# Kernel tuning notes

Hardware: AMD Instinct MI355X
Metric: run time of the kernel (lower is better)

Reference implementation:

```python
import jax, jax.numpy as jnp
import numpy as np

TIME_SEG_LEN = 5
PRED_STEPS = 1
B, N, D = 4, 4096, 4
F1, F2 = 32, 64  # cnn filters; F2 must equal GCSConv/Dense width 64


def _conv1d_time(x, Wc1, bc1, Wc2, bc2):
    # x: [B, N, T, D] -> per-node temporal CNN collapsing T=5 -> 1 -> [B, N, F2]
    b, n, t, d = x.shape
    xr = x.reshape(b * n, t, d)
    dn = ('NWC', 'WIO', 'NWC')
    h = jax.lax.conv_general_dilated(xr, Wc1, (1,), 'VALID', dimension_numbers=dn) + bc1
    h = jax.nn.relu(h)
    h = jax.lax.conv_general_dilated(h, Wc2, (1,), 'VALID', dimension_numbers=dn) + bc2
    return h.reshape(b, n, -1)  # [B, N, F2]


def setup_inputs() -> dict:
    key = jax.random.key(0)
    ks = jax.random.split(key, 12)
    time_segs = jax.random.normal(ks[0], (B, TIME_SEG_LEN, N, D), dtype=jnp.float32)
    edges = jax.random.randint(ks[1], (N, N), 0, 2, dtype=jnp.int32)
    s = lambda *sh: 1.0 / np.sqrt(sh[-2] if len(sh) > 1 else sh[0])
    return {
        'time_segs': time_segs,
        'edges': edges,
        'Wc1': jax.random.normal(ks[2], (3, D, F1), dtype=jnp.float32) * 0.3,
        'bc1': jnp.zeros((F1,), jnp.float32),
        'Wc2': jax.random.normal(ks[3], (3, F1, F2), dtype=jnp.float32) * 0.1,
        'bc2': jnp.zeros((F2,), jnp.float32),
        'Wg1': jax.random.normal(ks[4], (F2, 64), dtype=jnp.float32) * 0.125,
        'bg': jnp.zeros((64,), jnp.float32),
        'Wd': jax.random.normal(ks[5], (F2 + 64, 64), dtype=jnp.float32) * 0.09,
        'bd': jnp.zeros((64,), jnp.float32),
        'Wo': jax.random.normal(ks[6], (64, D), dtype=jnp.float32) * 0.125,
        'bo': jnp.zeros((D,), jnp.float32),
    }


def reference(time_segs, edges, Wc1, bc1, Wc2, bc2, Wg1, bg, Wd, bd, Wo, bo):
    A = edges.astype(jnp.float32)
    n = A.shape[0]
    deg = jnp.sum(A, axis=-1, keepdims=True)              # row degree
    A_norm = A / jnp.where(deg > 0, deg, 1.0)             # D^-1 A (symmetric=False)
    A_nd = A_norm * (1.0 - jnp.eye(n, dtype=A.dtype))     # self-edge masking of X row j == zeroing diag
    col_deg = jnp.sum(A, axis=0)                          # e = np.sum(edges, axis=0)
    alive = (col_deg != 0).astype(time_segs.dtype)[None, :, None]  # zero-degree nodes -> zeros branch

    ext = jnp.transpose(time_segs, (0, 2, 1, 3))          # [B, N, T, D]
    for i in range(PRED_STEPS):
        seg = ext[:, :, i:, :]                            # [B, N, 5, D]
        cond = _conv1d_time(seg, Wc1, bc1, Wc2, bc2)      # [B, N, F2]
        # Vectorized per-node masked GCSConv: row j of tanh(A X_j W1 + X_j W2 + b)
        # with X_j = X zeroed at node j. Skip term vanishes at row j.
        agg = jnp.einsum('jk,bkf->bjf', A_nd, cond)       # [B, N, F2]
        G = jnp.tanh(agg @ Wg1 + bg) * alive              # [B, N, 64]
        h = jax.nn.relu(jnp.concatenate([cond, G], axis=-1) @ Wd + bd)
        nxt = seg[:, :, -1, :] + jnp.tanh(h @ Wo + bo)    # residual update [B, N, D]
        ext = jnp.concatenate([ext, nxt[:, :, None, :]], axis=2)
    out = jnp.transpose(ext, (0, 2, 1, 3))                # [B, T+P, N, D]
    return out[:, TIME_SEG_LEN:, :, :]                    # [B, pred_steps, N, D]
```

## Files before the change

kernel.cpp:

```cpp
#include <hip/hip_runtime.h>
#include <math.h>

typedef unsigned short ushort_t;
typedef unsigned int uint_t;
typedef unsigned long long u64_t;
typedef __attribute__((ext_vector_type(8))) __bf16 bf16x8;
typedef __attribute__((ext_vector_type(4))) float f32x4;

#define NN 4096
#define TT 5
#define F1 32
#define F2 64

__device__ __forceinline__ ushort_t f2bf(float x) {
    union { float f; uint_t u; } v; v.f = x;
    uint_t r = (v.u + 0x7FFFu + ((v.u >> 16) & 1u)) >> 16;
    return (ushort_t)r;
}
__device__ __forceinline__ float bf16f(float x) {
    union { float f; uint_t u; } v; v.f = x;
    v.u = (v.u + 0x7FFFu + ((v.u >> 16) & 1u)) & 0xFFFF0000u;
    return v.f;
}
__device__ __forceinline__ uint_t pk2(float a, float b) {
    return (uint_t)f2bf(a) | ((uint_t)f2bf(b) << 16);
}
__device__ __forceinline__ float tanh_fast(float x) {
    const float xc = fminf(fmaxf(x, -10.f), 10.f);
    const float e = __expf(2.f * xc);
    return (e - 1.f) * __builtin_amdgcn_rcpf(e + 1.f);
}

#define H1S 104
#define CBS 80
__global__ __launch_bounds__(256) void k1_cond(
    const float* __restrict__ ts, const float* __restrict__ Wc1, const float* __restrict__ bc1,
    const float* __restrict__ Wc2, const float* __restrict__ bc2,
    float* __restrict__ condf, ushort_t* __restrict__ condT)
{
    const int b = blockIdx.y;
    const int j0 = blockIdx.x * 64;
    const int t = threadIdx.x;

    __shared__ float sWc1[384];
    __shared__ float sbc1[F1];
    __shared__ float sbc2[F2];
    __shared__ ushort_t sWc2T[64 * H1S];
    __shared__ ushort_t h1B[64 * H1S];
    __shared__ ushort_t scb[64 * CBS];

    for (int i = t; i < 384; i += 256) sWc1[i] = Wc1[i];
    if (t < F1) sbc1[t] = bc1[t];
    if (t < F2) sbc2[t] = bc2[t];
    for (int i = t; i < 96 * 64; i += 256) {
        const int e = i >> 6, f = i & 63;
        sWc2T[f * H1S + e] = f2bf(Wc2[i]);
    }
    __syncthreads();

    {
        const int n = t & 63, f10 = (t >> 6) * 8;
        const int j = j0 + n;
        float4 x[5];
        #pragma unroll
        for (int tt = 0; tt < 5; ++tt)
            x[tt] = *(const float4*)(ts + ((((size_t)b * TT + tt) << 12) + j) * 4);
        #pragma unroll
        for (int tt0 = 0; tt0 < 3; ++tt0) {
            #pragma unroll
            for (int ff = 0; ff < 8; ++ff) {
                const int f1 = f10 + ff;
                float a = sbc1[f1];
                #pragma unroll
                for (int dt = 0; dt < 3; ++dt) {
                    const float4 xx = x[tt0 + dt];
                    a += xx.x * sWc1[(dt * 4 + 0) * F1 + f1];
                    a += xx.y * sWc1[(dt * 4 + 1) * F1 + f1];
                    a += xx.z * sWc1[(dt * 4 + 2) * F1 + f1];
                    a += xx.w * sWc1[(dt * 4 + 3) * F1 + f1];
                }
                h1B[n * H1S + tt0 * 32 + f1] = f2bf(fmaxf(a, 0.f));
            }
        }
    }
    __syncthreads();

    {
        const int w = t >> 6, l = t & 63;
        const int m0 = w * 16, kseg = (l >> 4) * 8;
        f32x4 acc[4] = {};
        #pragma unroll
        for (int ks = 0; ks < 3; ++ks) {
            const bf16x8 av = *(const bf16x8*)&h1B[(m0 + (l & 15)) * H1S + ks * 32 + kseg];
            #pragma unroll
            for (int ct = 0; ct < 4; ++ct) {
                const bf16x8 bv = *(const bf16x8*)&sWc2T[(ct * 16 + (l & 15)) * H1S + ks * 32 + kseg];
                acc[ct] = __builtin_amdgcn_mfma_f32_16x16x32_bf16(av, bv, acc[ct], 0, 0, 0);
            }
        }
        #pragma unroll
        for (int ct = 0; ct < 4; ++ct)
            #pragma unroll
            for (int i = 0; i < 4; ++i) {
                const int row = m0 + (l >> 4) * 4 + i;
                const int col = ct * 16 + (l & 15);
                const float c = acc[ct][i] + sbc2[col];
                condf[((((size_t)b << 12) + j0 + row) << 6) + col] = c;
                scb[col * CBS + row] = f2bf(c);
            }
    }
    __syncthreads();
    {
        const int f2 = t >> 2, seg = t & 3;
        ushort_t* dst = condT + (((size_t)b * 64 + f2) << 12) + j0 + seg * 16;
        *(uint4*)dst = *(const uint4*)&scb[f2 * CBS + seg * 16];
        *(uint4*)(dst + 8) = *(const uint4*)&scb[f2 * CBS + seg * 16 + 8];
    }
}

__device__ __forceinline__ void stage_chunk(
    const int4 pa, int it, int kq, ushort_t* dstbuf, int soff, uint_t& regm, int& cnt)
{
    const u64_t b0 = __ballot(pa.x != 0);
    const u64_t b1 = __ballot(pa.y != 0);
    const u64_t b2 = __ballot(pa.z != 0);
    const u64_t b3 = __ballot(pa.w != 0);
    const uint_t m0 = (uint_t)(b0 | (b0 >> 32)), m1 = (uint_t)(b1 | (b1 >> 32));
    const uint_t m2 = (uint_t)(b2 | (b2 >> 32)), m3 = (uint_t)(b3 | (b3 >> 32));
    const uint_t nib = ((m0 >> kq) & 1u) | (((m1 >> kq) & 1u) << 1) |
                       (((m2 >> kq) & 1u) << 2) | (((m3 >> kq) & 1u) << 3);
    regm |= nib << (it * 4);
    cnt += (pa.x != 0) + (pa.y != 0) + (pa.z != 0) + (pa.w != 0);
    const uint_t h01 = (pa.x ? 0x3F80u : 0u) | (pa.y ? 0x3F800000u : 0u);
    const uint_t h23 = (pa.z ? 0x3F80u : 0u) | (pa.w ? 0x3F800000u : 0u);
    *(uint2*)(dstbuf + soff) = make_uint2(h01, h23);
}

__global__ __launch_bounds__(1024, 8) void k3_gemm(
    const int* __restrict__ edges, const ushort_t* __restrict__ condT,
    float* __restrict__ agg0, float* __restrict__ agg1,
    float* __restrict__ agg2, float* __restrict__ agg3,
    int* __restrict__ degI, uint_t* __restrict__ colbits)
{
    const int t = threadIdx.x;
    const int stripe = blockIdx.x >> 2, ks4 = blockIdx.x & 3;
    const int j0 = stripe * 32, kb = ks4 * 1024;

    __shared__ __align__(16) ushort_t abuf[8][4096];

    const int w = t >> 6, l = t & 63;
    const int r = t >> 5, kq = t & 31;
    const int rl = r & 15, rh = r >> 4;
    const int ks_s = kq >> 3, q_s = (kq >> 1) & 3;
    const int soff = (rh * 2048 + ks_s * 512 + (q_s * 16 + rl) * 8 + (kq & 1) * 4) ^ (q_s << 4);
    const int aoff = (l * 8) ^ ((l >> 4) << 4);

    const int* ep = edges + (size_t)(j0 + r) * NN + kb + kq * 4;
    const ushort_t* bp = condT + (size_t)(w * 16 + (l & 15)) * NN + kb + (l >> 4) * 8;

    uint_t regm = 0; int cnt = 0;
    int4 pa[4];

    #pragma unroll
    for (int c = 0; c < 4; ++c) pa[c] = *(const int4*)(ep + c * 128);
    #pragma unroll
    for (int c = 0; c < 4; ++c) stage_chunk(pa[c], c, kq, &abuf[c][0], soff, regm, cnt);
    __syncthreads();

    #pragma unroll
    for (int c = 0; c < 4; ++c) pa[c] = *(const int4*)(ep + (c + 4) * 128);

    f32x4 acc0 = {0.f, 0.f, 0.f, 0.f};
    f32x4 acc1 = {0.f, 0.f, 0.f, 0.f};

    #pragma unroll
    for (int ch = 0; ch < 4; ++ch) {
        const ushort_t* ab = &abuf[ch][0];
        const ushort_t* bpi = bp + ch * 128;
        #pragma unroll
        for (int ks = 0; ks < 4; ++ks) {
            const bf16x8 bfv = *(const bf16x8*)(bpi + ks * 32);
            const bf16x8 a0 = *(const bf16x8*)(ab + ks * 512 + aoff);
            const bf16x8 a1 = *(const bf16x8*)(ab + 2048 + ks * 512 + aoff);
            acc0 = __builtin_amdgcn_mfma_f32_16x16x32_bf16(a0, bfv, acc0, 0, 0, 0);
            acc1 = __builtin_amdgcn_mfma_f32_16x16x32_bf16(a1, bfv, acc1, 0, 0, 0);
        }
    }
    #pragma unroll
    for (int c = 0; c < 4; ++c) stage_chunk(pa[c], c + 4, kq, &abuf[c + 4][0], soff, regm, cnt);
    __syncthreads();

    #pragma unroll
    for (int ch = 4; ch < 8; ++ch) {
        const ushort_t* ab = &abuf[ch][0];
        const ushort_t* bpi = bp + ch * 128;
        #pragma unroll
        for (int ks = 0; ks < 4; ++ks) {
            const bf16x8 bfv = *(const bf16x8*)(bpi + ks * 32);
            const bf16x8 a0 = *(const bf16x8*)(ab + ks * 512 + aoff);
            const bf16x8 a1 = *(const bf16x8*)(ab + 2048 + ks * 512 + aoff);
            acc0 = __builtin_amdgcn_mfma_f32_16x16x32_bf16(a0, bfv, acc0, 0, 0, 0);
            acc1 = __builtin_amdgcn_mfma_f32_16x16x32_bf16(a1, bfv, acc1, 0, 0, 0);
        }
    }

    {
        float* aggS = (ks4 == 0) ? agg0 : (ks4 == 1) ? agg1 : (ks4 == 2) ? agg2 : agg3;
        const int col = w * 16 + (l & 15);
        float* dst = aggS + ((size_t)(col >> 6) * NN << 6) + (col & 63);
        #pragma unroll
        for (int i = 0; i < 4; ++i) {
            const int ja = j0 + (l >> 4) * 4 + i;
            dst[(size_t)ja << 6] = acc0[i];
            dst[(size_t)(ja + 16) << 6] = acc1[i];
        }
    }
    {
        int s = cnt;
        #pragma unroll
        for (int off = 16; off >= 1; off >>= 1) s += __shfl_down(s, off, 32);
        if (kq == 0) atomicAdd(&degI[j0 + r], s);
    }
    __syncthreads();
    uint_t* colsh = (uint_t*)&abuf[0][0];
    if (l < 32) colsh[w * 32 + kq] = regm;
    __syncthreads();
    if (t < 32) {
        uint_t v = 0;
        #pragma unroll
        for (int w2 = 0; w2 < 16; ++w2) v |= colsh[w2 * 32 + t];
        colsh[512 + t] = v;
    }
    __syncthreads();
    if (t < 32) {
        const int it = t >> 2, koct = t & 3;
        uint_t word = 0;
        #pragma unroll
        for (int s2 = 0; s2 < 8; ++s2)
            word |= ((colsh[512 + koct * 8 + s2] >> (it * 4)) & 15u) << (s2 * 4);
        atomicOr(&colbits[(kb >> 5) + t], word);
    }
}

#define WGS 88
#define WDS 136
#define HS  69
__global__ __launch_bounds__(256) void k4_mlp(
    const float* __restrict__ ts, const int* __restrict__ edges,
    const float* __restrict__ condf,
    const float* __restrict__ agg0, const float* __restrict__ agg1,
    const float* __restrict__ agg2, const float* __restrict__ agg3,
    const int* __restrict__ degI, const uint_t* __restrict__ colbits,
    const float* __restrict__ Wg1, const float* __restrict__ bg,
    const float* __restrict__ Wd, const float* __restrict__ bd,
    const float* __restrict__ Wo, const float* __restrict__ bo,
    float* __restrict__ out)
{
    const int b = blockIdx.y;
    const int j0 = blockIdx.x * 64;
    const int t = threadIdx.x;

    __shared__ ushort_t sWg1T[64 * WGS];
    __shared__ ushort_t sWdT[64 * WDS];
    __shared__ ushort_t aggB[64 * WGS];
    __shared__ ushort_t catB[64 * WDS];
    __shared__ float sH[64 * HS];
    __shared__ float sWo[256];
    __shared__ float sbg[64], sbd[64], sbo[4], sAlive[64];

    for (int i = t; i < 4096; i += 256) {
        const int in = i >> 6, o = i & 63;
        sWg1T[o * WGS + in] = f2bf(Wg1[i]);
    }
    for (int i = t; i < 8192; i += 256) {
        const int in = i >> 6, o = i & 63;
        sWdT[o * WDS + in] = f2bf(Wd[i]);
    }
    if (t < 256) sWo[t] = Wo[t];
    if (t < 64) { sbg[t] = bg[t]; sbd[t] = bd[t]; }
    if (t < 4) sbo[t] = bo[t];
    if (t < 64) {
        const int j = j0 + t;
        sAlive[t] = (float)((colbits[j >> 5] >> (j & 31)) & 1u);
    }
    {
        const int r = t >> 2, fs = t & 3;
        const int j = j0 + r;
        const float dv = (float)degI[j];
        const float inv = 1.f / (dv > 0.f ? dv : 1.f);
        const float dgf = edges[(size_t)j * NN + j] ? 1.f : 0.f;
        const size_t base = (((size_t)b << 12) + j) << 6;
        #pragma unroll
        for (int q = 0; q < 4; ++q) {
            const int f = fs * 16 + q * 4;
            const float4 a0 = *(const float4*)(agg0 + base + f);
            const float4 a1 = *(const float4*)(agg1 + base + f);
            const float4 a2 = *(const float4*)(agg2 + base + f);
            const float4 a3 = *(const float4*)(agg3 + base + f);
            const float4 c4 = *(const float4*)(condf + base + f);
            const float n0 = (a0.x + a1.x + a2.x + a3.x - dgf * bf16f(c4.x)) * inv;
            const float n1 = (a0.y + a1.y + a2.y + a3.y - dgf * bf16f(c4.y)) * inv;
            const float n2 = (a0.z + a1.z + a2.z + a3.z - dgf * bf16f(c4.z)) * inv;
            const float n3 = (a0.w + a1.w + a2.w + a3.w - dgf * bf16f(c4.w)) * inv;
            *(uint2*)&aggB[r * WGS + f] = make_uint2(pk2(n0, n1), pk2(n2, n3));
            *(uint2*)&catB[r * WDS + f] = make_uint2(pk2(c4.x, c4.y), pk2(c4.z, c4.w));
        }
    }
    __syncthreads();

    const int w = t >> 6, l = t & 63;
    const int m0 = w * 16, kseg = (l >> 4) * 8;

    {
        f32x4 acc[4] = {};
        #pragma unroll
        for (int ks = 0; ks < 2; ++ks) {
            const bf16x8 av = *(const bf16x8*)&aggB[(m0 + (l & 15)) * WGS + ks * 32 + kseg];
            #pragma unroll
            for (int ct = 0; ct < 4; ++ct) {
                const bf16x8 bv = *(const bf16x8*)&sWg1T[(ct * 16 + (l & 15)) * WGS + ks * 32 + kseg];
                acc[ct] = __builtin_amdgcn_mfma_f32_16x16x32_bf16(av, bv, acc[ct], 0, 0, 0);
            }
        }
        #pragma unroll
        for (int ct = 0; ct < 4; ++ct)
            #pragma unroll
            for (int i = 0; i < 4; ++i) {
                const int row = m0 + (l >> 4) * 4 + i;
                const int col = ct * 16 + (l & 15);
                const float g = tanh_fast(acc[ct][i] + sbg[col]) * sAlive[row];
                catB[row * WDS + 64 + col] = f2bf(g);
            }
    }
    __syncthreads();
    {
        f32x4 acc[4] = {};
        #pragma unroll
        for (int ks = 0; ks < 4; ++ks) {
            const bf16x8 av = *(const bf16x8*)&catB[(m0 + (l & 15)) * WDS + ks * 32 + kseg];
            #pragma unroll
            for (int ct = 0; ct < 4; ++ct) {
                const bf16x8 bv = *(const bf16x8*)&sWdT[(ct * 16 + (l & 15)) * WDS + ks * 32 + kseg];
                acc[ct] = __builtin_amdgcn_mfma_f32_16x16x32_bf16(av, bv, acc[ct], 0, 0, 0);
            }
        }
        #pragma unroll
        for (int ct = 0; ct < 4; ++ct)
            #pragma unroll
            for (int i = 0; i < 4; ++i) {
                const int row = m0 + (l >> 4) * 4 + i;
                const int col = ct * 16 + (l & 15);
                sH[row * HS + col] = fmaxf(acc[ct][i] + sbd[col], 0.f);
            }
    }
    __syncthreads();
    {
        const int r = t >> 2, d = t & 3;
        const int j = j0 + r;
        float s = sbo[d];
        #pragma unroll 8
        for (int f = 0; f < 64; ++f) s += sH[r * HS + f] * sWo[f * 4 + d];
        const float segl = ts[((((size_t)b * TT + 4) << 12) + j) * 4 + d];
        out[((((size_t)b << 12) + j) << 2) + d] = segl + tanh_fast(s);
    }
}

extern "C" void kernel_launch(void* const* d_in, const int* in_sizes, int n_in,
                              void* d_out, int out_size, void* d_ws, size_t ws_size,
                              hipStream_t stream)
{
    (void)in_sizes; (void)n_in; (void)out_size; (void)ws_size;
    const float* ts    = (const float*)d_in[0];
    const int*   edges = (const int*)d_in[1];
    const float* Wc1   = (const float*)d_in[2];
    const float* bc1   = (const float*)d_in[3];
    const float* Wc2   = (const float*)d_in[4];
    const float* bc2   = (const float*)d_in[5];
    const float* Wg1   = (const float*)d_in[6];
    const float* bg    = (const float*)d_in[7];
    const float* Wd    = (const float*)d_in[8];
    const float* bd    = (const float*)d_in[9];
    const float* Wo    = (const float*)d_in[10];
    const float* bo    = (const float*)d_in[11];
    float* out = (float*)d_out;

    char* ws = (char*)d_ws;
    ushort_t* condT   = (ushort_t*)(ws);
    float*    condf   = (float*)(ws + (size_t)(2 << 20));
    float*    agg0    = (float*)(ws + (size_t)(6 << 20));
    float*    agg1    = (float*)(ws + (size_t)(10 << 20));
    float*    agg2    = (float*)(ws + (size_t)(14 << 20));
    float*    agg3    = (float*)(ws + (size_t)(18 << 20));
    int*      degI    = (int*)(ws + (size_t)(22 << 20));
    uint_t*   colbits = (uint_t*)(ws + (size_t)(22 << 20) + 16384);

    hipMemsetAsync(degI, 0, 16384 + 512, stream);

    k1_cond<<<dim3(64, 4), 256, 0, stream>>>(ts, Wc1, bc1, Wc2, bc2, condf, condT);
    k3_gemm<<<512, 1024, 0, stream>>>(edges, condT, agg0, agg1, agg2, agg3, degI, colbits);
    k4_mlp<<<dim3(64, 4), 256, 0, stream>>>(ts, edges, condf, agg0, agg1, agg2, agg3,
                                            degI, colbits, Wg1, bg, Wd, bd, Wo, bo, out);
}
```

Baseline: 164.7 us.

## Fold memset into k1, double the block sizes, and prefetch B operands in the GEMM

```diff
diff --git a/kernel.cpp b/kernel.cpp
--- a/kernel.cpp
+++ b/kernel.cpp
@@ -30,13 +30,17 @@
     const float e = __expf(2.f * xc);
     return (e - 1.f) * __builtin_amdgcn_rcpf(e + 1.f);
 }
+__device__ __forceinline__ void lds_barrier() {
+    asm volatile("s_waitcnt lgkmcnt(0)\n\ts_barrier" ::: "memory");
+}
 
 #define H1S 104
 #define CBS 80
-__global__ __launch_bounds__(256) void k1_cond(
+__global__ __launch_bounds__(512) void k1_cond(
     const float* __restrict__ ts, const float* __restrict__ Wc1, const float* __restrict__ bc1,
     const float* __restrict__ Wc2, const float* __restrict__ bc2,
-    float* __restrict__ condf, ushort_t* __restrict__ condT)
+    float* __restrict__ condf, ushort_t* __restrict__ condT,
+    int* __restrict__ degI, uint_t* __restrict__ colbits)
 {
     const int b = blockIdx.y;
     const int j0 = blockIdx.x * 64;
@@ -49,61 +53,65 @@
     __shared__ ushort_t h1B[64 * H1S];
     __shared__ ushort_t scb[64 * CBS];
 
-    for (int i = t; i < 384; i += 256) sWc1[i] = Wc1[i];
+    if (blockIdx.x == 0 && b == 0) {
+        for (int i = t; i < 4096; i += 512) degI[i] = 0;
+        if (t < 128) colbits[t] = 0u;
+    }
+
+    for (int i = t; i < 384; i += 512) sWc1[i] = Wc1[i];
     if (t < F1) sbc1[t] = bc1[t];
     if (t < F2) sbc2[t] = bc2[t];
-    for (int i = t; i < 96 * 64; i += 256) {
+    for (int i = t; i < 96 * 64; i += 512) {
         const int e = i >> 6, f = i & 63;
         sWc2T[f * H1S + e] = f2bf(Wc2[i]);
     }
     __syncthreads();
 
     {
-        const int n = t & 63, f10 = (t >> 6) * 8;
+        const int n = t & 63, g = t >> 6;
         const int j = j0 + n;
         float4 x[5];
         #pragma unroll
         for (int tt = 0; tt < 5; ++tt)
             x[tt] = *(const float4*)(ts + ((((size_t)b * TT + tt) << 12) + j) * 4);
         #pragma unroll
-        for (int tt0 = 0; tt0 < 3; ++tt0) {
-            #pragma unroll
-            for (int ff = 0; ff < 8; ++ff) {
-                const int f1 = f10 + ff;
-                float a = sbc1[f1];
-                #pragma unroll
-                for (int dt = 0; dt < 3; ++dt) {
-                    const float4 xx = x[tt0 + dt];
-                    a += xx.x * sWc1[(dt * 4 + 0) * F1 + f1];
-                    a += xx.y * sWc1[(dt * 4 + 1) * F1 + f1];
-                    a += xx.z * sWc1[(dt * 4 + 2) * F1 + f1];
-                    a += xx.w * sWc1[(dt * 4 + 3) * F1 + f1];
-                }
-                h1B[n * H1S + tt0 * 32 + f1] = f2bf(fmaxf(a, 0.f));
-            }
+        for (int q = 0; q < 12; ++q) {
+            const int e = g * 12 + q;
+            const int tt0 = e >> 5, f1 = e & 31;
+            float a = sbc1[f1];
+            #pragma unroll
+            for (int dt = 0; dt < 3; ++dt) {
+                const float4 xx = x[tt0 + dt];
+                a += xx.x * sWc1[(dt * 4 + 0) * F1 + f1];
+                a += xx.y * sWc1[(dt * 4 + 1) * F1 + f1];
+                a += xx.z * sWc1[(dt * 4 + 2) * F1 + f1];
+                a += xx.w * sWc1[(dt * 4 + 3) * F1 + f1];
+            }
+            h1B[n * H1S + e] = f2bf(fmaxf(a, 0.f));
         }
     }
     __syncthreads();
 
     {
         const int w = t >> 6, l = t & 63;
-        const int m0 = w * 16, kseg = (l >> 4) * 8;
-        f32x4 acc[4] = {};
+        const int m0 = (w & 3) * 16, cH = (w >> 2) * 32;
+        const int kseg = (l >> 4) * 8;
+        f32x4 acc[2] = {};
         #pragma unroll
         for (int ks = 0; ks < 3; ++ks) {
             const bf16x8 av = *(const bf16x8*)&h1B[(m0 + (l & 15)) * H1S + ks * 32 + kseg];
             #pragma unroll
-            for (int ct = 0; ct < 4; ++ct) {
-                const bf16x8 bv = *(const bf16x8*)&sWc2T[(ct * 16 + (l & 15)) * H1S + ks * 32 + kseg];
+            for (int ct = 0; ct < 2; ++ct) {
+                const bf16x8 bv = *(const bf16x8*)&sWc2T[(cH + ct * 16 + (l & 15)) * H1S + ks * 32 + kseg];
                 acc[ct] = __builtin_amdgcn_mfma_f32_16x16x32_bf16(av, bv, acc[ct], 0, 0, 0);
             }
         }
         #pragma unroll
-        for (int ct = 0; ct < 4; ++ct)
+        for (int ct = 0; ct < 2; ++ct)
             #pragma unroll
             for (int i = 0; i < 4; ++i) {
                 const int row = m0 + (l >> 4) * 4 + i;
-                const int col = ct * 16 + (l & 15);
+                const int col = cH + ct * 16 + (l & 15);
                 const float c = acc[ct][i] + sbc2[col];
                 condf[((((size_t)b << 12) + j0 + row) << 6) + col] = c;
                 scb[col * CBS + row] = f2bf(c);
@@ -111,10 +119,9 @@
     }
     __syncthreads();
     {
-        const int f2 = t >> 2, seg = t & 3;
-        ushort_t* dst = condT + (((size_t)b * 64 + f2) << 12) + j0 + seg * 16;
-        *(uint4*)dst = *(const uint4*)&scb[f2 * CBS + seg * 16];
-        *(uint4*)(dst + 8) = *(const uint4*)&scb[f2 * CBS + seg * 16 + 8];
+        const int f2 = t >> 3, seg = t & 7;
+        ushort_t* dst = condT + (((size_t)b * 64 + f2) << 12) + j0 + seg * 8;
+        *(uint4*)dst = *(const uint4*)&scb[f2 * CBS + seg * 8];
     }
 }
 
@@ -160,12 +167,15 @@
 
     uint_t regm = 0; int cnt = 0;
     int4 pa[4];
+    bf16x8 bcur[4], bnxt[4];
 
     #pragma unroll
     for (int c = 0; c < 4; ++c) pa[c] = *(const int4*)(ep + c * 128);
     #pragma unroll
+    for (int ks = 0; ks < 4; ++ks) bcur[ks] = *(const bf16x8*)(bp + ks * 32);
+    #pragma unroll
     for (int c = 0; c < 4; ++c) stage_chunk(pa[c], c, kq, &abuf[c][0], soff, regm, cnt);
-    __syncthreads();
+    lds_barrier();
 
     #pragma unroll
     for (int c = 0; c < 4; ++c) pa[c] = *(const int4*)(ep + (c + 4) * 128);
@@ -175,32 +185,42 @@
 
     #pragma unroll
     for (int ch = 0; ch < 4; ++ch) {
+        const ushort_t* bpn = bp + (ch + 1) * 128;
+        #pragma unroll
+        for (int ks = 0; ks < 4; ++ks) bnxt[ks] = *(const bf16x8*)(bpn + ks * 32);
         const ushort_t* ab = &abuf[ch][0];
-        const ushort_t* bpi = bp + ch * 128;
         #pragma unroll
         for (int ks = 0; ks < 4; ++ks) {
-            const bf16x8 bfv = *(const bf16x8*)(bpi + ks * 32);
             const bf16x8 a0 = *(const bf16x8*)(ab + ks * 512 + aoff);
             const bf16x8 a1 = *(const bf16x8*)(ab + 2048 + ks * 512 + aoff);
-            acc0 = __builtin_amdgcn_mfma_f32_16x16x32_bf16(a0, bfv, acc0, 0, 0, 0);
-            acc1 = __builtin_amdgcn_mfma_f32_16x16x32_bf16(a1, bfv, acc1, 0, 0, 0);
-        }
+            acc0 = __builtin_amdgcn_mfma_f32_16x16x32_bf16(a0, bcur[ks], acc0, 0, 0, 0);
+            acc1 = __builtin_amdgcn_mfma_f32_16x16x32_bf16(a1, bcur[ks], acc1, 0, 0, 0);
+        }
+        #pragma unroll
+        for (int ks = 0; ks < 4; ++ks) bcur[ks] = bnxt[ks];
     }
     #pragma unroll
     for (int c = 0; c < 4; ++c) stage_chunk(pa[c], c + 4, kq, &abuf[c + 4][0], soff, regm, cnt);
-    __syncthreads();
+    lds_barrier();
 
     #pragma unroll
     for (int ch = 4; ch < 8; ++ch) {
+        if (ch < 7) {
+            const ushort_t* bpn = bp + (ch + 1) * 128;
+            #pragma unroll
+            for (int ks = 0; ks < 4; ++ks) bnxt[ks] = *(const bf16x8*)(bpn + ks * 32);
+        }
         const ushort_t* ab = &abuf[ch][0];
-        const ushort_t* bpi = bp + ch * 128;
         #pragma unroll
         for (int ks = 0; ks < 4; ++ks) {
-            const bf16x8 bfv = *(const bf16x8*)(bpi + ks * 32);
             const bf16x8 a0 = *(const bf16x8*)(ab + ks * 512 + aoff);
             const bf16x8 a1 = *(const bf16x8*)(ab + 2048 + ks * 512 + aoff);
-            acc0 = __builtin_amdgcn_mfma_f32_16x16x32_bf16(a0, bfv, acc0, 0, 0, 0);
-            acc1 = __builtin_amdgcn_mfma_f32_16x16x32_bf16(a1, bfv, acc1, 0, 0, 0);
+            acc0 = __builtin_amdgcn_mfma_f32_16x16x32_bf16(a0, bcur[ks], acc0, 0, 0, 0);
+            acc1 = __builtin_amdgcn_mfma_f32_16x16x32_bf16(a1, bcur[ks], acc1, 0, 0, 0);
+        }
+        if (ch < 7) {
+            #pragma unroll
+            for (int ks = 0; ks < 4; ++ks) bcur[ks] = bnxt[ks];
         }
     }
 
@@ -245,7 +265,7 @@
 #define WGS 88
 #define WDS 136
 #define HS  69
-__global__ __launch_bounds__(256) void k4_mlp(
+__global__ __launch_bounds__(512) void k4_mlp(
     const float* __restrict__ ts, const int* __restrict__ edges,
     const float* __restrict__ condf,
     const float* __restrict__ agg0, const float* __restrict__ agg1,
@@ -268,31 +288,31 @@
     __shared__ float sWo[256];
     __shared__ float sbg[64], sbd[64], sbo[4], sAlive[64];
 
-    for (int i = t; i < 4096; i += 256) {
+    for (int i = t; i < 4096; i += 512) {
         const int in = i >> 6, o = i & 63;
         sWg1T[o * WGS + in] = f2bf(Wg1[i]);
     }
-    for (int i = t; i < 8192; i += 256) {
+    for (int i = t; i < 8192; i += 512) {
         const int in = i >> 6, o = i & 63;
         sWdT[o * WDS + in] = f2bf(Wd[i]);
     }
     if (t < 256) sWo[t] = Wo[t];
-    if (t < 64) { sbg[t] = bg[t]; sbd[t] = bd[t]; }
-    if (t < 4) sbo[t] = bo[t];
-    if (t < 64) {
-        const int j = j0 + t;
-        sAlive[t] = (float)((colbits[j >> 5] >> (j & 31)) & 1u);
-    }
-    {
-        const int r = t >> 2, fs = t & 3;
+    if (t >= 256 && t < 320) { sbg[t - 256] = bg[t - 256]; sbd[t - 256] = bd[t - 256]; }
+    if (t >= 320 && t < 324) sbo[t - 320] = bo[t - 320];
+    if (t >= 384 && t < 448) {
+        const int j = j0 + t - 384;
+        sAlive[t - 384] = (float)((colbits[j >> 5] >> (j & 31)) & 1u);
+    }
+    {
+        const int r = t >> 3, fs = t & 7;
         const int j = j0 + r;
         const float dv = (float)degI[j];
         const float inv = 1.f / (dv > 0.f ? dv : 1.f);
         const float dgf = edges[(size_t)j * NN + j] ? 1.f : 0.f;
         const size_t base = (((size_t)b << 12) + j) << 6;
         #pragma unroll
-        for (int q = 0; q < 4; ++q) {
-            const int f = fs * 16 + q * 4;
+        for (int q = 0; q < 2; ++q) {
+            const int f = fs * 8 + q * 4;
             const float4 a0 = *(const float4*)(agg0 + base + f);
             const float4 a1 = *(const float4*)(agg1 + base + f);
             const float4 a2 = *(const float4*)(agg2 + base + f);
@@ -309,52 +329,53 @@
     __syncthreads();
 
     const int w = t >> 6, l = t & 63;
-    const int m0 = w * 16, kseg = (l >> 4) * 8;
-
-    {
-        f32x4 acc[4] = {};
+    const int m0 = (w & 3) * 16, cH = (w >> 2) * 32;
+    const int kseg = (l >> 4) * 8;
+
+    {
+        f32x4 acc[2] = {};
         #pragma unroll
         for (int ks = 0; ks < 2; ++ks) {
             const bf16x8 av = *(const bf16x8*)&aggB[(m0 + (l & 15)) * WGS + ks * 32 + kseg];
             #pragma unroll
-            for (int ct = 0; ct < 4; ++ct) {
-                const bf16x8 bv = *(const bf16x8*)&sWg1T[(ct * 16 + (l & 15)) * WGS + ks * 32 + kseg];
+            for (int ct = 0; ct < 2; ++ct) {
+                const bf16x8 bv = *(const bf16x8*)&sWg1T[(cH + ct * 16 + (l & 15)) * WGS + ks * 32 + kseg];
                 acc[ct] = __builtin_amdgcn_mfma_f32_16x16x32_bf16(av, bv, acc[ct], 0, 0, 0);
             }
         }
         #pragma unroll
-        for (int ct = 0; ct < 4; ++ct)
+        for (int ct = 0; ct < 2; ++ct)
             #pragma unroll
             for (int i = 0; i < 4; ++i) {
                 const int row = m0 + (l >> 4) * 4 + i;
-                const int col = ct * 16 + (l & 15);
+                const int col = cH + ct * 16 + (l & 15);
                 const float g = tanh_fast(acc[ct][i] + sbg[col]) * sAlive[row];
                 catB[row * WDS + 64 + col] = f2bf(g);
             }
     }
     __syncthreads();
     {
-        f32x4 acc[4] = {};
+        f32x4 acc[2] = {};
         #pragma unroll
         for (int ks = 0; ks < 4; ++ks) {
             const bf16x8 av = *(const bf16x8*)&catB[(m0 + (l & 15)) * WDS + ks * 32 + kseg];
             #pragma unroll
-            for (int ct = 0; ct < 4; ++ct) {
-                const bf16x8 bv = *(const bf16x8*)&sWdT[(ct * 16 + (l & 15)) * WDS + ks * 32 + kseg];
+            for (int ct = 0; ct < 2; ++ct) {
+                const bf16x8 bv = *(const bf16x8*)&sWdT[(cH + ct * 16 + (l & 15)) * WDS + ks * 32 + kseg];
                 acc[ct] = __builtin_amdgcn_mfma_f32_16x16x32_bf16(av, bv, acc[ct], 0, 0, 0);
             }
         }
         #pragma unroll
-        for (int ct = 0; ct < 4; ++ct)
+        for (int ct = 0; ct < 2; ++ct)
             #pragma unroll
             for (int i = 0; i < 4; ++i) {
                 const int row = m0 + (l >> 4) * 4 + i;
-                const int col = ct * 16 + (l & 15);
+                const int col = cH + ct * 16 + (l & 15);
                 sH[row * HS + col] = fmaxf(acc[ct][i] + sbd[col], 0.f);
             }
     }
     __syncthreads();
-    {
+    if (t < 256) {
         const int r = t >> 2, d = t & 3;
         const int j = j0 + r;
         float s = sbo[d];
@@ -394,10 +415,9 @@
     int*      degI    = (int*)(ws + (size_t)(22 << 20));
     uint_t*   colbits = (uint_t*)(ws + (size_t)(22 << 20) + 16384);
 
-    hipMemsetAsync(degI, 0, 16384 + 512, stream);
-
-    k1_cond<<<dim3(64, 4), 256, 0, stream>>>(ts, Wc1, bc1, Wc2, bc2, condf, condT);
+    k1_cond<<<dim3(64, 4), 512, 0, stream>>>(ts, Wc1, bc1, Wc2, bc2, condf, condT,
+                                             degI, colbits);
     k3_gemm<<<512, 1024, 0, stream>>>(edges, condT, agg0, agg1, agg2, agg3, degI, colbits);
-    k4_mlp<<<dim3(64, 4), 256, 0, stream>>>(ts, edges, condf, agg0, agg1, agg2, agg3,
+    k4_mlp<<<dim3(64, 4), 512, 0, stream>>>(ts, edges, condf, agg0, agg1, agg2, agg3,
                                             degI, colbits, Wg1, bg, Wd, bd, Wo, bo, out);
 }
```

After: 175.6 us. 1.07x slower.
